# Kernel optimization log

Hardware: AMD Instinct MI355X
Metric: run time of the kernel (lower is better)

## Reference

```python
import jax, jax.numpy as jnp
import numpy as np

B, T, E = 512, 12, 1024   # batch, channels/seq, embed_dim
NH, HS = 8, 128           # num_heads, head_size (head_size=128 hard-coded in source)
H = NH * HS               # sLSTM hidden = 1024 (== E)


def _layer_norm(x, g, b, eps=1e-5):
    mu = x.mean(-1, keepdims=True)
    var = x.var(-1, keepdims=True)
    return (x - mu) * jax.lax.rsqrt(var + eps) * g + b


def _conv1d_same(x, w, b):
    # x: (B, C, L), w: (O, I, K) odd K, 'same' padding, stride 1
    k = w.shape[-1]
    p = (k - 1) // 2
    y = jax.lax.conv_general_dilated(x, w, (1,), [(p, p)],
                                     dimension_numbers=('NCH', 'OIH', 'NCH'))
    return y + b[None, :, None]


def setup_inputs():
    key = jax.random.key(0)
    ks = jax.random.split(key, 16)
    s = 0.02
    def nrm(k, shape, scale=s):
        return jax.random.normal(k, shape, jnp.float32) * scale
    return {
        'x': jax.random.normal(ks[0], (B, T, E), jnp.float32),
        'ln_g': jnp.ones((E,), jnp.float32), 'ln_b': jnp.zeros((E,), jnp.float32),
        'fc1_w': nrm(ks[1], (12, 12, 3)), 'fc1_b': jnp.zeros((12,), jnp.float32),
        'fc2_w': nrm(ks[2], (12, 12)), 'fc2_b': jnp.zeros((12,), jnp.float32),
        'conv1_w': nrm(ks[3], (48, 12, 3)), 'conv1_b': jnp.zeros((48,), jnp.float32),
        'conv2_w': nrm(ks[4], (12, 48, 3)), 'conv2_b': jnp.zeros((12,), jnp.float32),
        'xl_ln_g': jnp.ones((E,), jnp.float32), 'xl_ln_b': jnp.zeros((E,), jnp.float32),
        'Wg': nrm(ks[5], (E, 4 * H)), 'bg': jnp.zeros((4 * H,), jnp.float32),
        'Rg': nrm(ks[6], (NH, 4 * HS, HS)),
        'gn_g': jnp.ones((H,), jnp.float32), 'gn_b': jnp.zeros((H,), jnp.float32),
        'upl_w': nrm(ks[7], (H, H)), 'upl_b': jnp.zeros((H,), jnp.float32),
        'upr_w': nrm(ks[8], (H, H)), 'upr_b': jnp.zeros((H,), jnp.float32),
        'down_w': nrm(ks[9], (H, E)), 'down_b': jnp.zeros((E,), jnp.float32),
    }


def _slstm_block(x, xl_ln_g, xl_ln_b, Wg, bg, Rg, gn_g, gn_b,
                 upl_w, upl_b, upr_w, upr_b, down_w, down_b):
    # Stabilized multi-head sLSTM block: pre-LN -> sLSTM recurrence (exp i/f gates
    # with max-stabilizer m), per-head GroupNorm, gated up/down proj (proj_factor=1),
    # residual. Recurrent weights are block-diagonal per head (NH, 4*HS, HS).
    xn = _layer_norm(x, xl_ln_g, xl_ln_b)
    gx = jnp.einsum('bte,eg->btg', xn, Wg) + bg            # (B,T,4H) input gate pre-acts
    gx = jnp.swapaxes(gx, 0, 1)                            # (T,B,4H)

    def step(carry, g_t):
        h, c, n, m = carry                                 # each (B,NH,HS)
        rec = jnp.einsum('bnh,ngh->bng', h, Rg)            # (B,NH,4HS)
        g = g_t.reshape(g_t.shape[0], NH, 4 * HS) + rec
        z_, i_, f_, o_ = jnp.split(g, 4, axis=-1)
        z = jnp.tanh(z_)
        o = jax.nn.sigmoid(o_)
        m_new = jnp.maximum(f_ + m, i_)                    # log-space stabilizer
        i = jnp.exp(i_ - m_new)
        f = jnp.exp(f_ + m - m_new)
        c = f * c + i * z
        n = f * n + i
        h = o * (c / n)
        return (h, c, n, m_new), h

    zero = jnp.zeros((x.shape[0], NH, HS), x.dtype)
    _, hseq = jax.lax.scan(step, (zero, zero, zero, zero), gx)
    h = jnp.swapaxes(hseq, 0, 1)                           # (B,T,NH,HS)
    # GroupNorm(num_groups=NH) over each head's HS channels
    mu = h.mean(-1, keepdims=True)
    var = h.var(-1, keepdims=True)
    hn = (h - mu) * jax.lax.rsqrt(var + 1e-5)
    hn = hn.reshape(x.shape[0], x.shape[1], H) * gn_g + gn_b
    left = jax.nn.gelu(hn @ upl_w + upl_b, approximate=False)
    right = hn @ upr_w + upr_b
    return (left * right) @ down_w + down_b + x


def reference(x, ln_g, ln_b, fc1_w, fc1_b, fc2_w, fc2_b, conv1_w, conv1_b,
              conv2_w, conv2_b, xl_ln_g, xl_ln_b, Wg, bg, Rg, gn_g, gn_b,
              upl_w, upl_b, upr_w, upr_b, down_w, down_b):
    xn = _layer_norm(x, ln_g, ln_b)
    skip = xn
    xc = _conv1d_same(xn, fc1_w, fc1_b)                    # fc1: Conv1d(12,12,3,'same')
    x1 = jnp.einsum('bcl,oc->bol', xc, fc2_w) + fc2_b[None, :, None]  # fc2: 1x1 conv
    x1 = _slstm_block(x1, xl_ln_g, xl_ln_b, Wg, bg, Rg, gn_g, gn_b,
                      upl_w, upl_b, upr_w, upr_b, down_w, down_b)
    # dropout(0.2) is identity in eval mode
    y = jax.nn.silu(xc) * x1 + skip
    z = _conv1d_same(y, conv1_w, conv1_b)                  # 12 -> 48
    z = _layer_norm(jax.nn.gelu(z, approximate=False), ln_g, ln_b)
    z = _conv1d_same(z, conv2_w, conv2_b)                  # 48 -> 12
    return z + skip
```

## Files before the change

### kernel.cpp

```cpp
#include <hip/hip_runtime.h>
#include <math.h>


typedef short short8_t __attribute__((ext_vector_type(8)));
typedef float floatx4 __attribute__((ext_vector_type(4)));
typedef float float2_t __attribute__((ext_vector_type(2)));

typedef unsigned int u32;
typedef const __attribute__((address_space(1))) u32 gu32;
typedef __attribute__((address_space(3))) u32 lu32;

static __device__ __forceinline__ float b2f(unsigned short u) {
    unsigned v = ((unsigned)u) << 16;
    return __builtin_bit_cast(float, v);
}
static __device__ __forceinline__ unsigned short f2b(float f) {
    unsigned u = __builtin_bit_cast(unsigned, f);
    u += 0x7FFFu + ((u >> 16) & 1u);
    return (unsigned short)(u >> 16);
}
static __device__ __forceinline__ float2_t make2u(unsigned u) {
    float2_t r;
    r.x = __builtin_bit_cast(float, u << 16);
    r.y = __builtin_bit_cast(float, u & 0xFFFF0000u);
    return r;
}
static __device__ __forceinline__ u32 pack2(float a, float b) {
    return ((u32)f2b(b) << 16) | (u32)f2b(a);
}
static __device__ __forceinline__ float gelu_fast(float x) {
    float u = 0.7978845608f * x * (1.f + 0.044715f * x * x);
    u = fminf(fmaxf(u, -9.f), 9.f);
    float e = __expf(2.f * u);
    float t = (e - 1.f) / (e + 1.f);
    return 0.5f * x * (1.f + t);
}


__global__ __launch_bounds__(256) void transpose_bf16_k(
    const float* __restrict__ src, unsigned short* __restrict__ dst, int K, int N)
{
    __shared__ unsigned short tl[32][33];
    const int n0 = blockIdx.x * 32, k0 = blockIdx.y * 32;
    const int tx = threadIdx.x & 31, ty = threadIdx.x >> 5;
#pragma unroll
    for (int r = 0; r < 4; r++) {
        int k = ty + r * 8;
        tl[tx][k] = f2b(src[(size_t)(k0 + k) * N + n0 + tx]);
    }
    __syncthreads();
#pragma unroll
    for (int r = 0; r < 4; r++) {
        int n = ty * 4 + r;
        dst[(size_t)(n0 + n) * K + k0 + tx] = tl[n][tx];
    }
}


template <int BF16OUT>
__global__ __launch_bounds__(256) void ln_kernel(
    const float* __restrict__ in, const float* __restrict__ g,
    const float* __restrict__ be, void* __restrict__ outp)
{
    const int row = blockIdx.x;
    const float* xr = in + (size_t)row * 1024;
    const int t = threadIdx.x;
    float v[4];
    float s = 0.f, ss = 0.f;
#pragma unroll
    for (int u = 0; u < 4; u++) {
        float q = xr[t + u * 256];
        v[u] = q; s += q; ss += q * q;
    }
#pragma unroll
    for (int off = 32; off >= 1; off >>= 1) {
        s += __shfl_xor(s, off);
        ss += __shfl_xor(ss, off);
    }
    __shared__ float red[8];
    const int wv = t >> 6, la = t & 63;
    if (la == 0) { red[wv] = s; red[4 + wv] = ss; }
    __syncthreads();
    s = red[0] + red[1] + red[2] + red[3];
    ss = red[4] + red[5] + red[6] + red[7];
    float mu = s * (1.f / 1024.f);
    float var = ss * (1.f / 1024.f) - mu * mu;
    float rs = rsqrtf(var + 1e-5f);
#pragma unroll
    for (int u = 0; u < 4; u++) {
        int i = t + u * 256;
        float yv = (v[u] - mu) * rs * g[i] + be[i];
        if (BF16OUT)
            ((unsigned short*)outp)[(size_t)row * 1024 + i] = f2b(yv);
        else
            ((float*)outp)[(size_t)row * 1024 + i] = yv;
    }
}


__global__ __launch_bounds__(256) void fc_kernel(
    const float* __restrict__ xn,
    const float* __restrict__ w1, const float* __restrict__ b1,
    const float* __restrict__ w2, const float* __restrict__ b2,
    float* __restrict__ xc, float* __restrict__ x1)
{
    const int t = threadIdx.x;
    const int gid = blockIdx.x * 256 + t;
    const int b = gid >> 10, l = gid & 1023;
    const float* xb = xn + (size_t)b * 12288;
    float inm[12], in0[12], inp[12];
#pragma unroll
    for (int ci = 0; ci < 12; ci++) {
        in0[ci] = xb[ci * 1024 + l];
        inm[ci] = (l > 0) ? xb[ci * 1024 + l - 1] : 0.f;
        inp[ci] = (l < 1023) ? xb[ci * 1024 + l + 1] : 0.f;
    }
    float xcv[12];
#pragma unroll
    for (int o = 0; o < 12; o++) {
        float a = b1[o];
#pragma unroll
        for (int ci = 0; ci < 12; ci++) {
            const float* wp = w1 + o * 36 + ci * 3;
            a += inm[ci] * wp[0] + in0[ci] * wp[1] + inp[ci] * wp[2];
        }
        xcv[o] = a;
        xc[(size_t)b * 12288 + o * 1024 + l] = a;
    }
#pragma unroll
    for (int o = 0; o < 12; o++) {
        float a = b2[o];
#pragma unroll
        for (int ci = 0; ci < 12; ci++) a += xcv[ci] * w2[o * 12 + ci];
        x1[(size_t)b * 12288 + o * 1024 + l] = a;
    }
}


template <int MODE>
__global__ __launch_bounds__(256) void gemm_kernel(
    const unsigned short* __restrict__ A, const unsigned short* __restrict__ BT,
    const float* __restrict__ bias, void* __restrict__ out,
    int M, int N, int K,
    const float* __restrict__ xc, const float* __restrict__ x1,
    const float* __restrict__ skip)
{
    __shared__ __align__(16) unsigned short sA[128 * 32];
    __shared__ __align__(16) unsigned short sB[128 * 32];
    const int t = threadIdx.x;
    const int m0 = blockIdx.y * 128;
    const int n0 = blockIdx.x * 128;
    const int w = t >> 6;
    const int lane = t & 63;
    const int wr = (w >> 1) * 64;
    const int wc = (w & 1) * 64;
    const int lrow = lane & 15;
    const int quad = lane >> 4;
    const int row_l = t >> 2;
    const int cs = (t & 3) * 8;

    const unsigned short* gA0 = A + (size_t)(m0 + row_l) * K + cs;
    const unsigned short* gA1 = A + (size_t)(m0 + row_l + 64) * K + cs;
    const unsigned short* gB0 = BT + (size_t)(n0 + row_l) * K + cs;
    const unsigned short* gB1 = BT + (size_t)(n0 + row_l + 64) * K + cs;
    unsigned short* lA0 = sA + w * 512;
    unsigned short* lA1 = sA + 2048 + w * 512;
    unsigned short* lB0 = sB + w * 512;
    unsigned short* lB1 = sB + 2048 + w * 512;

    floatx4 acc[4][4];
#pragma unroll
    for (int i = 0; i < 4; i++)
#pragma unroll
        for (int j = 0; j < 4; j++) acc[i][j] = (floatx4)0.f;

    for (int k0 = 0; k0 < K; k0 += 32) {
        __syncthreads();
        __builtin_amdgcn_global_load_lds((gu32*)(gA0 + k0), (lu32*)lA0, 16, 0, 0);
        __builtin_amdgcn_global_load_lds((gu32*)(gA1 + k0), (lu32*)lA1, 16, 0, 0);
        __builtin_amdgcn_global_load_lds((gu32*)(gB0 + k0), (lu32*)lB0, 16, 0, 0);
        __builtin_amdgcn_global_load_lds((gu32*)(gB1 + k0), (lu32*)lB1, 16, 0, 0);
        __syncthreads();
        short8_t af[4], bfr[4];
#pragma unroll
        for (int i = 0; i < 4; i++) {
            af[i] = *(const short8_t*)(sA + (wr + i * 16 + lrow) * 32 + quad * 8);
            bfr[i] = *(const short8_t*)(sB + (wc + i * 16 + lrow) * 32 + quad * 8);
        }
#pragma unroll
        for (int i = 0; i < 4; i++)
#pragma unroll
            for (int j = 0; j < 4; j++)
                acc[i][j] = __builtin_amdgcn_mfma_f32_16x16x32_bf16(
                    af[i], bfr[j], acc[i][j], 0, 0, 0);
    }

#pragma unroll
    for (int i = 0; i < 4; i++) {
#pragma unroll
        for (int j = 0; j < 4; j++) {
#pragma unroll
            for (int r = 0; r < 4; r++) {
                const int gm = m0 + wr + i * 16 + quad * 4 + r;
                const int gn = n0 + wc + j * 16 + lrow;
                const size_t idx = (size_t)gm * N + gn;
                float v = acc[i][j][r] + bias[gn];
                if (MODE == 0) {
                    ((unsigned short*)out)[idx] = f2b(v);
                } else {
                    float xcv = xc[idx];
                    float sig = xcv / (1.f + __expf(-xcv));
                    ((unsigned short*)out)[idx] =
                        f2b(sig * (v + x1[idx]) + skip[idx]);
                }
            }
        }
    }
}


#define RECP 516
#define HBP  136

__global__ __launch_bounds__(1024, 4) void slstm_rec_kernel(
    const float* __restrict__ Rg,
    const unsigned short* __restrict__ gxb,
    const float* __restrict__ gn_g, const float* __restrict__ gn_b,
    unsigned short* __restrict__ hnb)
{
    __shared__ __align__(16) float sRec[16 * RECP];
    __shared__ __align__(16) unsigned short sHb[16 * HBP];
    const int head = blockIdx.x;
    const int b0 = blockIdx.y * 16;
    const int t = threadIdx.x;
    const int w = t >> 6;
    const int lane = t & 63;
    const int quad = lane >> 4;
    const int l16 = lane & 15;

    short8_t Bf[2][4];
    {
        const float* Rh = Rg + (size_t)head * 65536;
#pragma unroll
        for (int jt = 0; jt < 2; jt++)
#pragma unroll
            for (int kk = 0; kk < 4; kk++) {
                const float* src =
                    Rh + (size_t)(w * 32 + jt * 16 + l16) * 128 + kk * 32 + quad * 8;
                short8_t v;
#pragma unroll
                for (int j = 0; j < 8; j++) v[j] = (short)f2b(src[j]);
                Bf[jt][kk] = v;
            }
    }

    for (int i = t; i < 16 * HBP; i += 1024) sHb[i] = 0;

    const int la = lane;
    float c0 = 0.f, n0s = 0.f, m0 = 0.f;
    float c1 = 0.f, n1s = 0.f, m1 = 0.f;
    const float gg0 = gn_g[head * 128 + la];
    const float gg1 = gn_g[head * 128 + la + 64];
    const float gb0 = gn_b[head * 128 + la];
    const float gb1 = gn_b[head * 128 + la + 64];

    __syncthreads();

    for (int step = 0; step < 12; step++) {
        const unsigned short* gp =
            gxb + ((size_t)(b0 + w) * 12 + step) * 4096 + head * 512;
        float gz0 = b2f(gp[la]),       gz1 = b2f(gp[64 + la]);
        float gi0 = b2f(gp[128 + la]), gi1 = b2f(gp[192 + la]);
        float gf0 = b2f(gp[256 + la]), gf1 = b2f(gp[320 + la]);
        float go0 = b2f(gp[384 + la]), go1 = b2f(gp[448 + la]);

        short8_t Af[4];
#pragma unroll
        for (int kk = 0; kk < 4; kk++)
            Af[kk] = *(const short8_t*)(sHb + l16 * HBP + kk * 32 + quad * 8);
        floatx4 D0 = (floatx4)0.f, D1 = (floatx4)0.f;
#pragma unroll
        for (int kk = 0; kk < 4; kk++) {
            D0 = __builtin_amdgcn_mfma_f32_16x16x32_bf16(Af[kk], Bf[0][kk], D0, 0, 0, 0);
            D1 = __builtin_amdgcn_mfma_f32_16x16x32_bf16(Af[kk], Bf[1][kk], D1, 0, 0, 0);
        }
#pragma unroll
        for (int r = 0; r < 4; r++) {
            sRec[(quad * 4 + r) * RECP + w * 32 + l16] = D0[r];
            sRec[(quad * 4 + r) * RECP + w * 32 + 16 + l16] = D1[r];
        }
        __syncthreads();

        const float* rr = sRec + w * RECP;
        float zp0 = gz0 + rr[la],       zp1 = gz1 + rr[64 + la];
        float ip0 = gi0 + rr[128 + la], ip1 = gi1 + rr[192 + la];
        float fp0 = gf0 + rr[256 + la], fp1 = gf1 + rr[320 + la];
        float op0 = go0 + rr[384 + la], op1 = go1 + rr[448 + la];

        float e20 = __expf(2.f * zp0), e21 = __expf(2.f * zp1);
        float z0 = (e20 - 1.f) / (e20 + 1.f), z1 = (e21 - 1.f) / (e21 + 1.f);
        float o0 = 1.f / (1.f + __expf(-op0)), o1 = 1.f / (1.f + __expf(-op1));
        float mn0 = fmaxf(fp0 + m0, ip0), mn1 = fmaxf(fp1 + m1, ip1);
        float ie0 = __expf(ip0 - mn0), ie1 = __expf(ip1 - mn1);
        float fe0 = __expf(fp0 + m0 - mn0), fe1 = __expf(fp1 + m1 - mn1);
        c0 = fe0 * c0 + ie0 * z0;  c1 = fe1 * c1 + ie1 * z1;
        n0s = fe0 * n0s + ie0;     n1s = fe1 * n1s + ie1;
        m0 = mn0;                  m1 = mn1;
        float h0 = o0 * (c0 / n0s), h1 = o1 * (c1 / n1s);

        float s = h0 + h1, ss = h0 * h0 + h1 * h1;
#pragma unroll
        for (int off = 32; off >= 1; off >>= 1) {
            s += __shfl_xor(s, off);
            ss += __shfl_xor(ss, off);
        }
        float mu = s * (1.f / 128.f);
        float var = ss * (1.f / 128.f) - mu * mu;
        float rs = rsqrtf(var + 1e-5f);
        size_t base = ((size_t)(b0 + w) * 12 + step) * 1024 + head * 128;
        hnb[base + la] = f2b((h0 - mu) * rs * gg0 + gb0);
        hnb[base + la + 64] = f2b((h1 - mu) * rs * gg1 + gb1);

        sHb[w * HBP + la] = f2b(h0);
        sHb[w * HBP + la + 64] = f2b(h1);
        __syncthreads();
    }
}


__global__ __launch_bounds__(256) void gate_kernel(
    const unsigned short* __restrict__ lr, unsigned short* __restrict__ glr)
{
    u32 pi = blockIdx.x * 256 + threadIdx.x;
    u32 m = pi >> 9, c = pi & 511;
    const u32* row = (const u32*)(lr + (size_t)m * 2048);
    float2_t lf = make2u(row[c]);
    float2_t rt = make2u(row[512 + c]);
    ((u32*)glr)[pi] = pack2(gelu_fast(lf.x) * rt.x, gelu_fast(lf.y) * rt.y);
}


__global__ __launch_bounds__(512, 6) void tail_fused_kernel(
    const unsigned short* __restrict__ y, const float* __restrict__ skip,
    const float* __restrict__ w1, const float* __restrict__ b1,
    const float* __restrict__ w2, const float* __restrict__ b2,
    const float* __restrict__ lng, const float* __restrict__ lnb,
    float* __restrict__ out)
{
    __shared__ unsigned short sY[12][1026];
    __shared__ unsigned short sZ[12][1026];
    __shared__ float sMR[12][2];
    const int b = blockIdx.x;
    const int t = threadIdx.x;
    const int p = t;
    const size_t boff = (size_t)b * 12288;

    {
        const u32* gy = (const u32*)(y + boff);
#pragma unroll
        for (int ci = 0; ci < 12; ci++)
            ((u32*)&sY[ci][0])[t] = gy[ci * 512 + t];
    }
    const float lgA = lng[2 * t], lbA = lnb[2 * t];
    const float lgB = lng[2 * t + 1], lbB = lnb[2 * t + 1];
    __syncthreads();

    float2_t acc[12];
#pragma unroll
    for (int o = 0; o < 12; o++) { float bv = b2[o]; acc[o] = float2_t{bv, bv}; }

    for (int q = 0; q < 4; q++) {
        float2_t a1[12];
#pragma unroll
        for (int o = 0; o < 12; o++) {
            float bo = b1[q * 12 + o];
            a1[o] = float2_t{bo, bo};
        }
        for (int ci = 0; ci < 12; ci++) {
            float2_t v0 = float2_t{b2f(sY[ci][p]), b2f(sY[ci][p + 512])};
            float2_t vm = float2_t{(p > 0) ? b2f(sY[ci][p - 1]) : 0.f,
                                   b2f(sY[ci][p + 511])};
            float2_t vp = float2_t{b2f(sY[ci][p + 1]),
                                   (p < 511) ? b2f(sY[ci][p + 513]) : 0.f};
            const float* wp = w1 + ci * 3;
#pragma unroll
            for (int o = 0; o < 12; o++) {
                const float* wo = wp + (q * 12 + o) * 36;
                a1[o] += vm * wo[0] + v0 * wo[1] + vp * wo[2];
            }
        }
#pragma unroll
        for (int o = 0; o < 12; o++) {
            sZ[o][p] = f2b(gelu_fast(a1[o].x));
            sZ[o][p + 512] = f2b(gelu_fast(a1[o].y));
        }
        __syncthreads();

        {
            const int wv = t >> 6, la = t & 63;
#pragma unroll
            for (int j = 0; j < 2; j++) {
                const int ch = wv + j * 8;
                if (ch < 12) {
                    float s = 0.f, ss = 0.f;
#pragma unroll
                    for (int u = 0; u < 8; u++) {
                        float2_t v = make2u(((const u32*)&sZ[ch][0])[la + u * 64]);
                        s += v.x + v.y;
                        ss += v.x * v.x + v.y * v.y;
                    }
#pragma unroll
                    for (int off = 32; off >= 1; off >>= 1) {
                        s += __shfl_xor(s, off);
                        ss += __shfl_xor(ss, off);
                    }
                    if (la == 0) {
                        float mu = s * (1.f / 1024.f);
                        float var = ss * (1.f / 1024.f) - mu * mu;
                        sMR[ch][0] = mu;
                        sMR[ch][1] = rsqrtf(var + 1e-5f);
                    }
                }
            }
        }
        __syncthreads();

#pragma unroll
        for (int ch = 0; ch < 12; ch++) {
            const float mu = sMR[ch][0], rs = sMR[ch][1];
            float2_t f = make2u(((const u32*)&sZ[ch][0])[t]);
            f.x = (f.x - mu) * rs * lgA + lbA;
            f.y = (f.y - mu) * rs * lgB + lbB;
            ((u32*)&sZ[ch][0])[t] = pack2(f.x, f.y);
        }
        __syncthreads();

        for (int ci = 0; ci < 12; ci++) {
            float2_t z0 = float2_t{b2f(sZ[ci][p]), b2f(sZ[ci][p + 512])};
            float2_t zm = float2_t{(p > 0) ? b2f(sZ[ci][p - 1]) : 0.f,
                                   b2f(sZ[ci][p + 511])};
            float2_t zp = float2_t{b2f(sZ[ci][p + 1]),
                                   (p < 511) ? b2f(sZ[ci][p + 513]) : 0.f};
            const float* wp = w2 + (q * 12 + ci) * 3;
#pragma unroll
            for (int o = 0; o < 12; o++)
                acc[o] += zm * wp[o * 144] + z0 * wp[o * 144 + 1]
                        + zp * wp[o * 144 + 2];
        }
        __syncthreads();
    }

#pragma unroll
    for (int o = 0; o < 12; o++) {
        size_t i0 = boff + (size_t)o * 1024 + p;
        out[i0] = acc[o].x + skip[i0];
        out[i0 + 512] = acc[o].y + skip[i0 + 512];
    }
}


extern "C" void kernel_launch(void* const* d_in, const int* in_sizes, int n_in,
                              void* d_out, int out_size, void* d_ws, size_t ws_size,
                              hipStream_t stream)
{
    (void)in_sizes; (void)n_in; (void)out_size; (void)ws_size;
    const float* x      = (const float*)d_in[0];
    const float* ln_g   = (const float*)d_in[1];
    const float* ln_b   = (const float*)d_in[2];
    const float* fc1_w  = (const float*)d_in[3];
    const float* fc1_b  = (const float*)d_in[4];
    const float* fc2_w  = (const float*)d_in[5];
    const float* fc2_b  = (const float*)d_in[6];
    const float* conv1_w= (const float*)d_in[7];
    const float* conv1_b= (const float*)d_in[8];
    const float* conv2_w= (const float*)d_in[9];
    const float* conv2_b= (const float*)d_in[10];
    const float* xl_g   = (const float*)d_in[11];
    const float* xl_b   = (const float*)d_in[12];
    const float* Wg     = (const float*)d_in[13];
    const float* bg     = (const float*)d_in[14];
    const float* Rg     = (const float*)d_in[15];
    const float* gn_g   = (const float*)d_in[16];
    const float* gn_b   = (const float*)d_in[17];
    const float* upl_w  = (const float*)d_in[18];
    const float* upl_b  = (const float*)d_in[19];
    const float* upr_w  = (const float*)d_in[20];
    const float* upr_b  = (const float*)d_in[21];
    const float* down_w = (const float*)d_in[22];
    const float* down_b = (const float*)d_in[23];

    char* ws = (char*)d_ws;
    size_t off = 0;
    auto alloc = [&](size_t bytes) -> char* {
        char* p = ws + off;
        off = (off + bytes + 255) & ~(size_t)255;
        return p;
    };
    float* xn            = (float*)alloc(25165824);
    float* xc            = (float*)alloc(25165824);
    float* x1            = (float*)alloc(25165824);
    unsigned short* xn2b = (unsigned short*)alloc(12582912);
    unsigned short* gxb  = (unsigned short*)alloc(50331648);
    unsigned short* hnb  = (unsigned short*)alloc(12582912);
    unsigned short* lrb  = (unsigned short*)alloc(25165824);
    unsigned short* glrb = (unsigned short*)alloc(12582912);
    unsigned short* yb   = (unsigned short*)alloc(12582912);
    unsigned short* WgT  = (unsigned short*)alloc(8388608);
    unsigned short* WupT = (unsigned short*)alloc(4194304);
    unsigned short* WdT  = (unsigned short*)alloc(2097152);
    float* bup           = (float*)alloc(8192);

    transpose_bf16_k<<<dim3(128, 32), 256, 0, stream>>>(Wg, WgT, 1024, 4096);
    transpose_bf16_k<<<dim3(32, 32), 256, 0, stream>>>(upl_w, WupT, 1024, 1024);
    transpose_bf16_k<<<dim3(32, 32), 256, 0, stream>>>(upr_w, WupT + 1024 * 1024, 1024, 1024);
    transpose_bf16_k<<<dim3(32, 32), 256, 0, stream>>>(down_w, WdT, 1024, 1024);
    {
        hipMemcpyAsync(bup, upl_b, 4096, hipMemcpyDeviceToDevice, stream);
        hipMemcpyAsync(bup + 1024, upr_b, 4096, hipMemcpyDeviceToDevice, stream);
    }

    ln_kernel<0><<<6144, 256, 0, stream>>>(x, ln_g, ln_b, xn);
    fc_kernel<<<2048, 256, 0, stream>>>(xn, fc1_w, fc1_b, fc2_w, fc2_b, xc, x1);
    ln_kernel<1><<<6144, 256, 0, stream>>>(x1, xl_g, xl_b, xn2b);
    gemm_kernel<0><<<dim3(32, 48), 256, 0, stream>>>(
        xn2b, WgT, bg, gxb, 6144, 4096, 1024, nullptr, nullptr, nullptr);
    slstm_rec_kernel<<<dim3(8, 32), 1024, 0, stream>>>(Rg, gxb, gn_g, gn_b, hnb);
    gemm_kernel<0><<<dim3(16, 48), 256, 0, stream>>>(
        hnb, WupT, bup, lrb, 6144, 2048, 1024, nullptr, nullptr, nullptr);
    gate_kernel<<<12288, 256, 0, stream>>>(lrb, glrb);
    gemm_kernel<2><<<dim3(8, 48), 256, 0, stream>>>(
        glrb, WdT, down_b, yb, 6144, 1024, 1024, xc, x1, xn);
    tail_fused_kernel<<<512, 512, 0, stream>>>(
        yb, xn, conv1_w, conv1_b, conv2_w, conv2_b, ln_g, ln_b, (float*)d_out);
}
```

Before: 465.9 us.

## Use fast reciprocal intrinsics and widen tail kernel to one column per thread

Replaces IEEE divisions in gelu, silu and the sLSTM gate math with hardware reciprocal (rcpf) and rewrites tanh as a sigmoid form, aiming to cut the cost of division sequences. The tail fused conv/LN/conv kernel moves from 512 threads handling two columns each to 1024 threads handling one column each. Zero-padded shared rows replace the boundary branches, and the per-channel LN statistics now use one wave per channel. This exposes more parallelism per block, at the cost of slightly lower precision and possibly higher register pressure under the tighter launch bounds.

Measured after the change: 557.3 us. 1.2x slower.

```diff
diff --git a/kernel.cpp b/kernel.cpp
--- a/kernel.cpp
+++ b/kernel.cpp
@@ -31,9 +31,7 @@
 static __device__ __forceinline__ float gelu_fast(float x) {
     float u = 0.7978845608f * x * (1.f + 0.044715f * x * x);
     u = fminf(fmaxf(u, -9.f), 9.f);
-    float e = __expf(2.f * u);
-    float t = (e - 1.f) / (e + 1.f);
-    return 0.5f * x * (1.f + t);
+    return x * __builtin_amdgcn_rcpf(1.f + __expf(-2.f * u));
 }
 
 
@@ -209,7 +207,7 @@
                     ((unsigned short*)out)[idx] = f2b(v);
                 } else {
                     float xcv = xc[idx];
-                    float sig = xcv / (1.f + __expf(-xcv));
+                    float sig = xcv * __builtin_amdgcn_rcpf(1.f + __expf(-xcv));
                     ((unsigned short*)out)[idx] =
                         f2b(sig * (v + x1[idx]) + skip[idx]);
                 }
@@ -297,16 +295,19 @@
         float fp0 = gf0 + rr[256 + la], fp1 = gf1 + rr[320 + la];
         float op0 = go0 + rr[384 + la], op1 = go1 + rr[448 + la];
 
-        float e20 = __expf(2.f * zp0), e21 = __expf(2.f * zp1);
-        float z0 = (e20 - 1.f) / (e20 + 1.f), z1 = (e21 - 1.f) / (e21 + 1.f);
-        float o0 = 1.f / (1.f + __expf(-op0)), o1 = 1.f / (1.f + __expf(-op1));
+        float e20 = __expf(-2.f * zp0), e21 = __expf(-2.f * zp1);
+        float z0 = 2.f * __builtin_amdgcn_rcpf(1.f + e20) - 1.f;
+        float z1 = 2.f * __builtin_amdgcn_rcpf(1.f + e21) - 1.f;
+        float o0 = __builtin_amdgcn_rcpf(1.f + __expf(-op0));
+        float o1 = __builtin_amdgcn_rcpf(1.f + __expf(-op1));
         float mn0 = fmaxf(fp0 + m0, ip0), mn1 = fmaxf(fp1 + m1, ip1);
         float ie0 = __expf(ip0 - mn0), ie1 = __expf(ip1 - mn1);
         float fe0 = __expf(fp0 + m0 - mn0), fe1 = __expf(fp1 + m1 - mn1);
         c0 = fe0 * c0 + ie0 * z0;  c1 = fe1 * c1 + ie1 * z1;
         n0s = fe0 * n0s + ie0;     n1s = fe1 * n1s + ie1;
         m0 = mn0;                  m1 = mn1;
-        float h0 = o0 * (c0 / n0s), h1 = o1 * (c1 / n1s);
+        float h0 = o0 * c0 * __builtin_amdgcn_rcpf(n0s);
+        float h1 = o1 * c1 * __builtin_amdgcn_rcpf(n1s);
 
         float s = h0 + h1, ss = h0 * h0 + h1 * h1;
 #pragma unroll
@@ -340,48 +341,49 @@
 }
 
 
-__global__ __launch_bounds__(512, 6) void tail_fused_kernel(
+__global__ __launch_bounds__(1024, 8) void tail_fused_kernel(
     const unsigned short* __restrict__ y, const float* __restrict__ skip,
     const float* __restrict__ w1, const float* __restrict__ b1,
     const float* __restrict__ w2, const float* __restrict__ b2,
     const float* __restrict__ lng, const float* __restrict__ lnb,
     float* __restrict__ out)
 {
-    __shared__ unsigned short sY[12][1026];
-    __shared__ unsigned short sZ[12][1026];
+    __shared__ unsigned short sYr[2 + 12 * 1026];
+    __shared__ unsigned short sZr[2 + 12 * 1026];
     __shared__ float sMR[12][2];
     const int b = blockIdx.x;
     const int t = threadIdx.x;
-    const int p = t;
     const size_t boff = (size_t)b * 12288;
 
+    if (t < 2) { sYr[t] = 0; sZr[t] = 0; }
+    if (t < 12) {
+        sYr[2 + t * 1026 + 1024] = 0; sYr[2 + t * 1026 + 1025] = 0;
+        sZr[2 + t * 1026 + 1024] = 0; sZr[2 + t * 1026 + 1025] = 0;
+    }
     {
         const u32* gy = (const u32*)(y + boff);
-#pragma unroll
-        for (int ci = 0; ci < 12; ci++)
-            ((u32*)&sY[ci][0])[t] = gy[ci * 512 + t];
-    }
-    const float lgA = lng[2 * t], lbA = lnb[2 * t];
-    const float lgB = lng[2 * t + 1], lbB = lnb[2 * t + 1];
+        for (int i = t; i < 6144; i += 1024) {
+            int ci = i >> 9, c = i & 511;
+            ((u32*)(sYr + 2 + ci * 1026))[c] = gy[i];
+        }
+    }
+    const int dci0 = t >> 9;
+    const int dc = t & 511;
+    const float lgA = lng[2 * dc], lbA = lnb[2 * dc];
+    const float lgB = lng[2 * dc + 1], lbB = lnb[2 * dc + 1];
     __syncthreads();
 
-    float2_t acc[12];
-#pragma unroll
-    for (int o = 0; o < 12; o++) { float bv = b2[o]; acc[o] = float2_t{bv, bv}; }
+    float acc[12];
+#pragma unroll
+    for (int o = 0; o < 12; o++) acc[o] = b2[o];
 
     for (int q = 0; q < 4; q++) {
-        float2_t a1[12];
-#pragma unroll
-        for (int o = 0; o < 12; o++) {
-            float bo = b1[q * 12 + o];
-            a1[o] = float2_t{bo, bo};
-        }
+        float a1[12];
+#pragma unroll
+        for (int o = 0; o < 12; o++) a1[o] = b1[q * 12 + o];
         for (int ci = 0; ci < 12; ci++) {
-            float2_t v0 = float2_t{b2f(sY[ci][p]), b2f(sY[ci][p + 512])};
-            float2_t vm = float2_t{(p > 0) ? b2f(sY[ci][p - 1]) : 0.f,
-                                   b2f(sY[ci][p + 511])};
-            float2_t vp = float2_t{b2f(sY[ci][p + 1]),
-                                   (p < 511) ? b2f(sY[ci][p + 513]) : 0.f};
+            const unsigned short* r = sYr + 2 + ci * 1026 + t;
+            float vm = b2f(r[-1]), v0 = b2f(r[0]), vp = b2f(r[1]);
             const float* wp = w1 + ci * 3;
 #pragma unroll
             for (int o = 0; o < 12; o++) {
@@ -390,57 +392,51 @@
             }
         }
 #pragma unroll
-        for (int o = 0; o < 12; o++) {
-            sZ[o][p] = f2b(gelu_fast(a1[o].x));
-            sZ[o][p + 512] = f2b(gelu_fast(a1[o].y));
-        }
+        for (int o = 0; o < 12; o++)
+            sZr[2 + o * 1026 + t] = f2b(gelu_fast(a1[o]));
         __syncthreads();
 
         {
             const int wv = t >> 6, la = t & 63;
-#pragma unroll
-            for (int j = 0; j < 2; j++) {
-                const int ch = wv + j * 8;
-                if (ch < 12) {
-                    float s = 0.f, ss = 0.f;
-#pragma unroll
-                    for (int u = 0; u < 8; u++) {
-                        float2_t v = make2u(((const u32*)&sZ[ch][0])[la + u * 64]);
-                        s += v.x + v.y;
-                        ss += v.x * v.x + v.y * v.y;
-                    }
-#pragma unroll
-                    for (int off = 32; off >= 1; off >>= 1) {
-                        s += __shfl_xor(s, off);
-                        ss += __shfl_xor(ss, off);
-                    }
-                    if (la == 0) {
-                        float mu = s * (1.f / 1024.f);
-                        float var = ss * (1.f / 1024.f) - mu * mu;
-                        sMR[ch][0] = mu;
-                        sMR[ch][1] = rsqrtf(var + 1e-5f);
-                    }
+            if (wv < 12) {
+                const u32* zr = (const u32*)(sZr + 2 + wv * 1026);
+                float s = 0.f, ss = 0.f;
+#pragma unroll
+                for (int u = 0; u < 8; u++) {
+                    float2_t v = make2u(zr[la + u * 64]);
+                    s += v.x + v.y;
+                    ss += v.x * v.x + v.y * v.y;
+                }
+#pragma unroll
+                for (int off = 32; off >= 1; off >>= 1) {
+                    s += __shfl_xor(s, off);
+                    ss += __shfl_xor(ss, off);
+                }
+                if (la == 0) {
+                    float mu = s * (1.f / 1024.f);
+                    float var = ss * (1.f / 1024.f) - mu * mu;
+                    sMR[wv][0] = mu;
+                    sMR[wv][1] = rsqrtf(var + 1e-5f);
                 }
             }
         }
         __syncthreads();
 
 #pragma unroll
-        for (int ch = 0; ch < 12; ch++) {
+        for (int u = 0; u < 6; u++) {
+            const int ch = dci0 + 2 * u;
             const float mu = sMR[ch][0], rs = sMR[ch][1];
-            float2_t f = make2u(((const u32*)&sZ[ch][0])[t]);
+            u32* zr = (u32*)(sZr + 2 + ch * 1026);
+            float2_t f = make2u(zr[dc]);
             f.x = (f.x - mu) * rs * lgA + lbA;
             f.y = (f.y - mu) * rs * lgB + lbB;
-            ((u32*)&sZ[ch][0])[t] = pack2(f.x, f.y);
+            zr[dc] = pack2(f.x, f.y);
         }
         __syncthreads();
 
         for (int ci = 0; ci < 12; ci++) {
-            float2_t z0 = float2_t{b2f(sZ[ci][p]), b2f(sZ[ci][p + 512])};
-            float2_t zm = float2_t{(p > 0) ? b2f(sZ[ci][p - 1]) : 0.f,
-                                   b2f(sZ[ci][p + 511])};
-            float2_t zp = float2_t{b2f(sZ[ci][p + 1]),
-                                   (p < 511) ? b2f(sZ[ci][p + 513]) : 0.f};
+            const unsigned short* r = sZr + 2 + ci * 1026 + t;
+            float zm = b2f(r[-1]), z0 = b2f(r[0]), zp = b2f(r[1]);
             const float* wp = w2 + (q * 12 + ci) * 3;
 #pragma unroll
             for (int o = 0; o < 12; o++)
@@ -452,9 +448,8 @@
 
 #pragma unroll
     for (int o = 0; o < 12; o++) {
-        size_t i0 = boff + (size_t)o * 1024 + p;
-        out[i0] = acc[o].x + skip[i0];
-        out[i0 + 512] = acc[o].y + skip[i0 + 512];
+        size_t i0 = boff + (size_t)o * 1024 + t;
+        out[i0] = acc[o] + skip[i0];
     }
 }
 
@@ -530,6 +525,6 @@
     gate_kernel<<<12288, 256, 0, stream>>>(lrb, glrb);
     gemm_kernel<2><<<dim3(8, 48), 256, 0, stream>>>(
         glrb, WdT, down_b, yb, 6144, 1024, 1024, xc, x1, xn);
-    tail_fused_kernel<<<512, 512, 0, stream>>>(
+    tail_fused_kernel<<<512, 1024, 0, stream>>>(
         yb, xn, conv1_w, conv1_b, conv2_w, conv2_b, ln_g, ln_b, (float*)d_out);
 }
```
